# Kernel optimization log

Measured on AMD Instinct MI355X. Metric: run time of the kernel, lower is better.

Reference implementation:

```python
import jax, jax.numpy as jnp
import numpy as np

N, D, C, S = 100000, 512, 4096, 50000


def setup_inputs() -> dict:
    key = jax.random.key(0)
    k1, k2 = jax.random.split(key)
    X = jax.random.normal(k1, (N, D), dtype=jnp.float32)
    codebook_sum = jax.random.normal(k2, (C, D), dtype=jnp.float32)
    prompt_mask = jnp.arange(N) < S  # first S rows are support (True), rest are queries
    return {"X": X, "codebook_sum": codebook_sum, "prompt_mask": prompt_mask, "num_support": S}


def reference(X, codebook_sum, prompt_mask, num_support):
    # num_support is a static Python int (replaces torch.nonzero(prompt_mask) dynamic split)
    s = num_support
    support = X[:s]                                   # [S, D] support (prompt_mask==True)
    query = X[s:]                                     # [Q, D] queries (prompt_mask==False)
    # dense similarity matmul + top-1 nearest-codebook search + gather
    cos_sim = jnp.einsum('sd,cd->sc', support, codebook_sum)  # [S, C]
    top_idx = jnp.argmax(cos_sim, axis=1)             # [S]
    code_n = codebook_sum[top_idx]                    # [S, D] gathered nearest codes
    # mean-pooled prototypes broadcast over queries
    proto = jnp.mean(support, axis=0)                 # [D]
    proto_code = jnp.mean(code_n, axis=0)             # [D]
    # euclidean distances to each prototype
    query_score = jnp.sqrt(jnp.sum((query - proto) ** 2, axis=1))        # [Q]
    query_score_code = jnp.sqrt(jnp.sum((query - proto_code) ** 2, axis=1))  # [Q]
    return (query_score + query_score_code) / 2
```

## Files before the change

kernel.cpp:

```cpp
#include <hip/hip_runtime.h>
#include <hip/hip_bf16.h>

#define NTOT 100000
#define DIM  512
#define CB   4096
#define SSUP 50000
#define NQ   (NTOT - SSUP)

#define MTILES 391
#define MPAD   (MTILES * 128)
#define NTILES 32

typedef __bf16 bf16x8 __attribute__((ext_vector_type(8)));
typedef __bf16 bf16x4 __attribute__((ext_vector_type(4)));
typedef float  f32x4  __attribute__((ext_vector_type(4)));

#define OFF_CBBF   0
#define OFF_XB     4194304
#define OFF_PV     55443456
#define OFF_PI     61849600
#define OFF_PSUM   68255744
#define OFF_PCSUM  68257792
#define OFF_HIST   68259840
#define OFF_TIDX   68276224
#define WS_NEED    (68276224 + 200000)
#define ZERO_BYTES (2048 + 2048 + 16384)

#define F_OFF_PSUM   4194304
#define F_OFF_PCSUM  4196352
#define F_OFF_HIST   4198400
#define F_OFF_TIDX   4214784

__device__ __forceinline__ void load_lds16(const void* g, void* l) {
    __builtin_amdgcn_global_load_lds(
        (const __attribute__((address_space(1))) void*)g,
        (__attribute__((address_space(3))) void*)l, 16, 0, 0);
}

__global__ void k_convert(const float* __restrict__ src, __bf16* __restrict__ dst) {
    int i = (blockIdx.x * 256 + threadIdx.x) * 4;
    float4 v = *(const float4*)(src + i);
    bf16x4 o;
    o[0] = (__bf16)v.x; o[1] = (__bf16)v.y; o[2] = (__bf16)v.z; o[3] = (__bf16)v.w;
    *(bf16x4*)(dst + i) = o;
}

__global__ void k_proto_sum(const float* __restrict__ X, float* __restrict__ protoSum) {
    const int d = threadIdx.x;
    const int r0 = blockIdx.x * 500;
    float acc = 0.f;
    for (int r = r0; r < r0 + 500; ++r)
        acc += X[(size_t)r * DIM + d];
    atomicAdd(&protoSum[d], acc);
}

__global__ __launch_bounds__(256)
void k_gemm_tile(const __bf16* __restrict__ Xb, const __bf16* __restrict__ cbb,
                 float* __restrict__ pv, int* __restrict__ pi)
{
    __shared__ __bf16 lA[128 * 32];
    __shared__ __bf16 lB[128 * 32];
    __shared__ float  sv[128][2];
    __shared__ int    si[128][2];

    const int tid  = threadIdx.x;
    const int wave = tid >> 6;
    const int lane = tid & 63;
    const int wm   = wave >> 1;
    const int wn   = wave & 1;
    const int l15  = lane & 15;
    const int q    = lane >> 4;
    const int nt   = blockIdx.x;
    const int mt   = blockIdx.y;
    const size_t r0 = (size_t)mt * 128;
    const int    c0 = nt * 128;

    f32x4 acc[4][4];
    #pragma unroll
    for (int i = 0; i < 4; ++i)
        #pragma unroll
        for (int j = 0; j < 4; ++j)
            acc[i][j] = (f32x4){0.f, 0.f, 0.f, 0.f};

    for (int k0 = 0; k0 < 512; k0 += 32) {
        __syncthreads();
        #pragma unroll
        for (int i = 0; i < 2; ++i) {
            const int ck  = i * 256 + tid;
            const int row = ck >> 2;
            const int kc  = ck & 3;
            load_lds16(Xb  + (r0 + row) * DIM + k0 + kc * 8, lA + ck * 8);
            load_lds16(cbb + (size_t)(c0 + row) * DIM + k0 + kc * 8, lB + ck * 8);
        }
        __syncthreads();

        bf16x8 af[4], bfr[4];
        #pragma unroll
        for (int t = 0; t < 4; ++t) {
            af[t]  = *(const bf16x8*)(lA + (wm * 64 + t * 16 + l15) * 32 + q * 8);
            bfr[t] = *(const bf16x8*)(lB + (wn * 64 + t * 16 + l15) * 32 + q * 8);
        }
        #pragma unroll
        for (int tm = 0; tm < 4; ++tm)
            #pragma unroll
            for (int tn = 0; tn < 4; ++tn)
                acc[tm][tn] = __builtin_amdgcn_mfma_f32_16x16x32_bf16(
                    af[tm], bfr[tn], acc[tm][tn], 0, 0, 0);
    }

    #pragma unroll
    for (int tm = 0; tm < 4; ++tm) {
        #pragma unroll
        for (int reg = 0; reg < 4; ++reg) {
            float v = -3.0e38f; int idx = 0;
            #pragma unroll
            for (int tn = 0; tn < 4; ++tn) {
                float x = acc[tm][tn][reg];
                int   c = c0 + wn * 64 + tn * 16 + l15;
                if (x > v) { v = x; idx = c; }
            }
            #pragma unroll
            for (int off = 1; off < 16; off <<= 1) {
                float ov = __shfl_xor(v, off, 64);
                int   oi = __shfl_xor(idx, off, 64);
                if (ov > v) { v = ov; idx = oi; }
            }
            if (l15 == 0) {
                int rl = wm * 64 + tm * 16 + q * 4 + reg;
                sv[rl][wn] = v;
                si[rl][wn] = idx;
            }
        }
    }
    __syncthreads();
    if (tid < 128) {
        float v0 = sv[tid][0], v1 = sv[tid][1];
        size_t r = r0 + tid;
        pv[r * 32 + nt] = fmaxf(v0, v1);
        pi[r * 32 + nt] = (v1 > v0) ? si[tid][1] : si[tid][0];
    }
}

__global__ void k_argmax_reduce(const float* __restrict__ pv, const int* __restrict__ pi,
                                int* __restrict__ top_idx) {
    int r = blockIdx.x * 256 + threadIdx.x;
    if (r >= SSUP) return;
    float v = -3.0e38f; int idx = 0;
    #pragma unroll 8
    for (int j = 0; j < 32; ++j) {
        float x = pv[(size_t)r * 32 + j];
        if (x > v) { v = x; idx = pi[(size_t)r * 32 + j]; }
    }
    top_idx[r] = idx;
}

__global__ __launch_bounds__(256, 2)
void k_gemm_argmax(const float* __restrict__ X, const __bf16* __restrict__ cbb,
                   int* __restrict__ top_idx)
{
    __shared__ float redv[64][2];
    __shared__ int   redi[64][2];

    const int tid  = threadIdx.x;
    const int wave = tid >> 6;
    const int lane = tid & 63;
    const int wm   = wave >> 1;
    const int wn   = wave & 1;
    const int l15  = lane & 15;
    const int q    = lane >> 4;
    const int r0   = blockIdx.x * 64;

    bf16x8 aflat[2][16];
    #pragma unroll
    for (int tm = 0; tm < 2; ++tm) {
        const int r = r0 + wm * 32 + tm * 16 + l15;
        const bool valid = (r < SSUP);
        const float* xr = X + (size_t)r * DIM + q * 8;
        #pragma unroll
        for (int kt = 0; kt < 16; ++kt) {
            float4 v0, v1;
            if (valid) {
                v0 = *(const float4*)(xr + kt * 32);
                v1 = *(const float4*)(xr + kt * 32 + 4);
            } else {
                v0 = make_float4(0.f, 0.f, 0.f, 0.f);
                v1 = v0;
            }
            bf16x8 f;
            f[0] = (__bf16)v0.x; f[1] = (__bf16)v0.y; f[2] = (__bf16)v0.z; f[3] = (__bf16)v0.w;
            f[4] = (__bf16)v1.x; f[5] = (__bf16)v1.y; f[6] = (__bf16)v1.z; f[7] = (__bf16)v1.w;
            aflat[tm][kt] = f;
        }
    }

    float mx[8];
    int   mi[8];
    #pragma unroll
    for (int i = 0; i < 8; ++i) { mx[i] = -3.0e38f; mi[i] = 0; }
    const f32x4 zero4 = {0.f, 0.f, 0.f, 0.f};

    for (int ct = 0; ct < 32; ++ct) {
        const int c0 = ct * 128 + wn * 64;
        const __bf16* bptr[4];
        #pragma unroll
        for (int tn = 0; tn < 4; ++tn)
            bptr[tn] = cbb + (size_t)(c0 + tn * 16 + l15) * DIM + q * 8;

        f32x4 acc[2][4];
        #pragma unroll
        for (int i = 0; i < 2; ++i)
            #pragma unroll
            for (int j = 0; j < 4; ++j)
                acc[i][j] = zero4;

        #pragma unroll
        for (int kt = 0; kt < 16; ++kt) {
            bf16x8 b[4];
            #pragma unroll
            for (int tn = 0; tn < 4; ++tn)
                b[tn] = *(const bf16x8*)(bptr[tn] + kt * 32);
            #pragma unroll
            for (int tm = 0; tm < 2; ++tm)
                #pragma unroll
                for (int tn = 0; tn < 4; ++tn)
                    acc[tm][tn] = __builtin_amdgcn_mfma_f32_16x16x32_bf16(
                        aflat[tm][kt], b[tn], acc[tm][tn], 0, 0, 0);
        }
        #pragma unroll
        for (int tm = 0; tm < 2; ++tm)
            #pragma unroll
            for (int tn = 0; tn < 4; ++tn)
                #pragma unroll
                for (int reg = 0; reg < 4; ++reg) {
                    float v = acc[tm][tn][reg];
                    int slot = tm * 4 + reg;
                    int col  = c0 + tn * 16 + l15;
                    if (v > mx[slot]) { mx[slot] = v; mi[slot] = col; }
                }
    }

    #pragma unroll
    for (int slot = 0; slot < 8; ++slot) {
        float v  = mx[slot];
        int  idx = mi[slot];
        #pragma unroll
        for (int off = 1; off < 16; off <<= 1) {
            float ov = __shfl_xor(v, off, 64);
            int   oi = __shfl_xor(idx, off, 64);
            if (ov > v) { v = ov; idx = oi; }
        }
        if (l15 == 0) {
            int rowl = wm * 32 + (slot >> 2) * 16 + q * 4 + (slot & 3);
            redv[rowl][wn] = v;
            redi[rowl][wn] = idx;
        }
    }
    __syncthreads();
    if (tid < 64) {
        int r = r0 + tid;
        if (r < SSUP) {
            float v0 = redv[tid][0], v1 = redv[tid][1];
            top_idx[r] = (v1 > v0) ? redi[tid][1] : redi[tid][0];
        }
    }
}

__global__ void k_hist(const int* __restrict__ top_idx, int* __restrict__ hist) {
    __shared__ int lh[CB];
    for (int i = threadIdx.x; i < CB; i += blockDim.x) lh[i] = 0;
    __syncthreads();
    for (int i = blockIdx.x * blockDim.x + threadIdx.x; i < SSUP; i += gridDim.x * blockDim.x)
        atomicAdd(&lh[top_idx[i]], 1);
    __syncthreads();
    for (int i = threadIdx.x; i < CB; i += blockDim.x) {
        int v = lh[i];
        if (v) atomicAdd(&hist[i], v);
    }
}

__global__ void k_proto_code(const float* __restrict__ cb, const int* __restrict__ hist,
                             float* __restrict__ pcSum) {
    const int d  = threadIdx.x;
    const int c0 = blockIdx.x * 64;
    float acc = 0.f;
    for (int c = c0; c < c0 + 64; ++c) {
        float w = (float)hist[c];
        if (w != 0.f) acc += w * cb[(size_t)c * DIM + d];
    }
    atomicAdd(&pcSum[d], acc);
}

__global__ void k_query(const float* __restrict__ X, const float* __restrict__ protoSum,
                        const float* __restrict__ pcSum, float* __restrict__ out) {
    const int lane   = threadIdx.x & 63;
    const int waveId = (blockIdx.x * blockDim.x + threadIdx.x) >> 6;
    const int nwaves = (gridDim.x * blockDim.x) >> 6;
    const float invS = 1.0f / (float)SSUP;

    for (int r = waveId; r < NQ; r += nwaves) {
        const float* xr = X + (size_t)(SSUP + r) * DIM;
        float s1 = 0.f, s2 = 0.f;
        #pragma unroll
        for (int i = 0; i < 2; ++i) {
            int dd = lane * 4 + i * 256;
            float4 xq = *(const float4*)(xr + dd);
            float4 p  = *(const float4*)(protoSum + dd);
            float4 pc = *(const float4*)(pcSum + dd);
            float d0, d1, d2, d3;
            d0 = xq.x - p.x * invS; d1 = xq.y - p.y * invS;
            d2 = xq.z - p.z * invS; d3 = xq.w - p.w * invS;
            s1 += d0 * d0 + d1 * d1 + d2 * d2 + d3 * d3;
            d0 = xq.x - pc.x * invS; d1 = xq.y - pc.y * invS;
            d2 = xq.z - pc.z * invS; d3 = xq.w - pc.w * invS;
            s2 += d0 * d0 + d1 * d1 + d2 * d2 + d3 * d3;
        }
        #pragma unroll
        for (int off = 32; off > 0; off >>= 1) {
            s1 += __shfl_xor(s1, off, 64);
            s2 += __shfl_xor(s2, off, 64);
        }
        if (lane == 0)
            out[r] = 0.5f * (sqrtf(s1) + sqrtf(s2));
    }
}

extern "C" void kernel_launch(void* const* d_in, const int* in_sizes, int n_in,
                              void* d_out, int out_size, void* d_ws, size_t ws_size,
                              hipStream_t stream) {
    const float* X  = (const float*)d_in[0];
    const float* cb = (const float*)d_in[1];
    float* out = (float*)d_out;
    char* ws = (char*)d_ws;

    __bf16* cbb = (__bf16*)(ws + OFF_CBBF);

    if (ws_size >= (size_t)WS_NEED) {
        __bf16* Xb       = (__bf16*)(ws + OFF_XB);
        float*  pv       = (float*)(ws + OFF_PV);
        int*    pi       = (int*)(ws + OFF_PI);
        float*  protoSum = (float*)(ws + OFF_PSUM);
        float*  pcSum    = (float*)(ws + OFF_PCSUM);
        int*    hist     = (int*)(ws + OFF_HIST);
        int*    top_idx  = (int*)(ws + OFF_TIDX);

        hipMemsetAsync(ws + OFF_PSUM, 0, ZERO_BYTES, stream);

        k_convert<<<(CB * DIM) / 1024, 256, 0, stream>>>(cb, cbb);
        k_convert<<<(MPAD * DIM) / 1024, 256, 0, stream>>>(X, Xb);
        k_proto_sum<<<100, 512, 0, stream>>>(X, protoSum);

        dim3 grid(NTILES, MTILES);
        k_gemm_tile<<<grid, 256, 0, stream>>>(Xb, cbb, pv, pi);

        k_argmax_reduce<<<(SSUP + 255) / 256, 256, 0, stream>>>(pv, pi, top_idx);
        k_hist<<<64, 256, 0, stream>>>(top_idx, hist);
        k_proto_code<<<CB / 64, 512, 0, stream>>>(cb, hist, pcSum);
        k_query<<<1024, 256, 0, stream>>>(X, protoSum, pcSum, out);
    } else {
        float*  protoSum = (float*)(ws + F_OFF_PSUM);
        float*  pcSum    = (float*)(ws + F_OFF_PCSUM);
        int*    hist     = (int*)(ws + F_OFF_HIST);
        int*    top_idx  = (int*)(ws + F_OFF_TIDX);

        hipMemsetAsync(ws + F_OFF_PSUM, 0, ZERO_BYTES, stream);

        k_convert<<<(CB * DIM) / 1024, 256, 0, stream>>>(cb, cbb);
        k_proto_sum<<<100, 512, 0, stream>>>(X, protoSum);
        k_gemm_argmax<<<(SSUP + 63) / 64, 256, 0, stream>>>(X, cbb, top_idx);
        k_hist<<<64, 256, 0, stream>>>(top_idx, hist);
        k_proto_code<<<CB / 64, 512, 0, stream>>>(cb, hist, pcSum);
        k_query<<<1024, 256, 0, stream>>>(X, protoSum, pcSum, out);
    }
}
```

Baseline: 621.9 us.

## Replace GEMM with 256x256 software-pipelined swizzled MFMA kernel and fuse convert+protosum

Replaces the 128x128 single-buffered GEMM with a 256x256-tile, 8-wave kernel. It double-buffers K-slices of 64 in a 128KB LDS using direct global-to-LDS loads with an XOR swizzle, and interleaves loads with MFMA quads under explicit waitcnt and barrier control plus setprio. The bf16 conversion of X is fused with the support-row prototype sum, so X is read once in that stage. The argmax partials shrink to 16 per row. The change aims to raise MFMA utilisation and cut global and LDS traffic, but it adds heavy manual synchronisation and a large LDS footprint that limits occupancy.

```diff
diff --git a/kernel.cpp b/kernel.cpp
--- a/kernel.cpp
+++ b/kernel.cpp
@@ -7,9 +7,9 @@
 #define SSUP 50000
 #define NQ   (NTOT - SSUP)
 
-#define MTILES 391
-#define MPAD   (MTILES * 128)
-#define NTILES 32
+#define MT2   196
+#define MPAD2 (MT2 * 256)
+#define NT2   16
 
 typedef __bf16 bf16x8 __attribute__((ext_vector_type(8)));
 typedef __bf16 bf16x4 __attribute__((ext_vector_type(4)));
@@ -17,13 +17,13 @@
 
 #define OFF_CBBF   0
 #define OFF_XB     4194304
-#define OFF_PV     55443456
-#define OFF_PI     61849600
-#define OFF_PSUM   68255744
-#define OFF_PCSUM  68257792
-#define OFF_HIST   68259840
-#define OFF_TIDX   68276224
-#define WS_NEED    (68276224 + 200000)
+#define OFF_PV     55574528
+#define OFF_PI     58785792
+#define OFF_PSUM   61997056
+#define OFF_PCSUM  61999104
+#define OFF_HIST   62001152
+#define OFF_TIDX   62017536
+#define WS_NEED    (62017536 + 200000)
 #define ZERO_BYTES (2048 + 2048 + 16384)
 
 #define F_OFF_PSUM   4194304
@@ -36,6 +36,11 @@
         (const __attribute__((address_space(1))) void*)g,
         (__attribute__((address_space(3))) void*)l, 16, 0, 0);
 }
+
+#define BARRIER() __builtin_amdgcn_s_barrier()
+#define LGKM0()   do { asm volatile("s_waitcnt lgkmcnt(0)" ::: "memory"); \
+                       __builtin_amdgcn_sched_barrier(0); } while (0)
+#define VMC(N)    asm volatile("s_waitcnt vmcnt(" #N ")" ::: "memory")
 
 __global__ void k_convert(const float* __restrict__ src, __bf16* __restrict__ dst) {
     int i = (blockIdx.x * 256 + threadIdx.x) * 4;
@@ -43,6 +48,287 @@
     bf16x4 o;
     o[0] = (__bf16)v.x; o[1] = (__bf16)v.y; o[2] = (__bf16)v.z; o[3] = (__bf16)v.w;
     *(bf16x4*)(dst + i) = o;
+}
+
+__global__ __launch_bounds__(256)
+void k_conv_psum(const float* __restrict__ X, __bf16* __restrict__ Xb,
+                 float* __restrict__ protoSum)
+{
+    __shared__ float red[4][512];
+    const int tid  = threadIdx.x;
+    const int c8   = (tid & 63) * 8;
+    const int rsub = tid >> 6;
+    const size_t rbase = (size_t)blockIdx.x * 512 + rsub;
+
+    float acc[8];
+    #pragma unroll
+    for (int j = 0; j < 8; ++j) acc[j] = 0.f;
+
+    for (int r = 0; r < 512; r += 4) {
+        const size_t row = rbase + r;
+        const float* p = X + row * DIM + c8;
+        float4 v0 = *(const float4*)p;
+        float4 v1 = *(const float4*)(p + 4);
+        bf16x8 o;
+        o[0] = (__bf16)v0.x; o[1] = (__bf16)v0.y; o[2] = (__bf16)v0.z; o[3] = (__bf16)v0.w;
+        o[4] = (__bf16)v1.x; o[5] = (__bf16)v1.y; o[6] = (__bf16)v1.z; o[7] = (__bf16)v1.w;
+        *(bf16x8*)(Xb + row * DIM + c8) = o;
+        if (row < SSUP) {
+            acc[0] += v0.x; acc[1] += v0.y; acc[2] += v0.z; acc[3] += v0.w;
+            acc[4] += v1.x; acc[5] += v1.y; acc[6] += v1.z; acc[7] += v1.w;
+        }
+    }
+    #pragma unroll
+    for (int j = 0; j < 8; ++j) red[rsub][c8 + j] = acc[j];
+    __syncthreads();
+    if (rsub == 0) {
+        #pragma unroll
+        for (int j = 0; j < 8; ++j)
+            atomicAdd(&protoSum[c8 + j],
+                      red[0][c8 + j] + red[1][c8 + j] + red[2][c8 + j] + red[3][c8 + j]);
+    }
+}
+
+
+__device__ __forceinline__ void stage_half(const __bf16* __restrict__ g, size_t grow0,
+                                           int k0, char* ldsop, int half, int tid)
+{
+    char* dst = ldsop + half * 16384;
+    #pragma unroll
+    for (int i = 0; i < 2; ++i) {
+        const int ck  = i * 512 + tid;
+        const int row = ck >> 3;
+        const int sc  = (ck & 7) ^ (row & 7);
+        load_lds16(g + (grow0 + (size_t)row) * DIM + k0 + sc * 8, dst + ck * 16);
+    }
+}
+
+template<int BUFOFF, int MH>
+__device__ __forceinline__ void ds_load_A(const char* aptr, int off0, int off1,
+                                          bf16x8 (&a)[4][2])
+{
+    #pragma unroll
+    for (int t = 0; t < 4; ++t) {
+        const char* p = aptr + BUFOFF + MH * 8192 + t * 2048;
+        a[t][0] = *(const bf16x8*)(p + off0);
+        a[t][1] = *(const bf16x8*)(p + off1);
+    }
+}
+
+template<int BUFOFF, int NH>
+__device__ __forceinline__ void ds_load_B(const char* bptr, int off0, int off1,
+                                          bf16x8 (&b)[2][2])
+{
+    #pragma unroll
+    for (int n = 0; n < 2; ++n) {
+        const char* p = bptr + BUFOFF + NH * 4096 + n * 2048;
+        b[n][0] = *(const bf16x8*)(p + off0);
+        b[n][1] = *(const bf16x8*)(p + off1);
+    }
+}
+
+template<int MH, int NH>
+__device__ __forceinline__ void mfma_quad(const bf16x8 (&a)[4][2], const bf16x8 (&b)[2][2],
+                                          f32x4 (&acc)[8][4])
+{
+    __builtin_amdgcn_s_setprio(1);
+    #pragma unroll
+    for (int t = 0; t < 4; ++t)
+        #pragma unroll
+        for (int n = 0; n < 2; ++n)
+            #pragma unroll
+            for (int ks = 0; ks < 2; ++ks)
+                acc[MH * 4 + t][NH * 2 + n] = __builtin_amdgcn_mfma_f32_16x16x32_bf16(
+                    a[t][ks], b[n][ks], acc[MH * 4 + t][NH * 2 + n], 0, 0, 0);
+    __builtin_amdgcn_s_setprio(0);
+    __builtin_amdgcn_sched_barrier(0);
+}
+
+__global__ __launch_bounds__(512, 2)
+void k_gemm256(const __bf16* __restrict__ Xb, const __bf16* __restrict__ cbb,
+               float* __restrict__ pv, int* __restrict__ pi)
+{
+    __shared__ __align__(16) char lds[131072];
+
+    const int tid  = threadIdx.x;
+    const int lane = tid & 63;
+    const int wid  = tid >> 6;
+    const int wm   = wid >> 2;
+    const int wn   = wid & 3;
+    const int l15  = lane & 15;
+    const int q    = lane >> 4;
+    const int nt   = blockIdx.x;
+    const int mt   = blockIdx.y;
+    const size_t r0  = (size_t)mt * 256;
+    const size_t c0g = (size_t)nt * 256;
+
+    const int off0 = l15 * 128 + ((q)     ^ (l15 & 7)) * 16;
+    const int off1 = l15 * 128 + ((4 + q) ^ (l15 & 7)) * 16;
+    const char* aptr = lds + wm * 16384;
+    const char* bptr = lds + wn * 8192;
+
+    f32x4 acc[8][4];
+    #pragma unroll
+    for (int i = 0; i < 8; ++i)
+        #pragma unroll
+        for (int j = 0; j < 4; ++j)
+            acc[i][j] = (f32x4){0.f, 0.f, 0.f, 0.f};
+
+    bf16x8 a[4][2], b0[2][2], b1[2][2];
+
+    stage_half(Xb,  r0,        0,  lds + 0,     0, tid);
+    stage_half(Xb,  r0 + 128,  0,  lds + 0,     1, tid);
+    stage_half(cbb, c0g,       0,  lds + 32768, 0, tid);
+    stage_half(cbb, c0g + 128, 0,  lds + 32768, 1, tid);
+    stage_half(cbb, c0g,       64, lds + 98304, 0, tid);
+    stage_half(cbb, c0g + 128, 64, lds + 98304, 1, tid);
+    VMC(4);
+    BARRIER();
+
+    #pragma unroll 1
+    for (int it = 0; it < 3; ++it) {
+        const int kA1 = (2 * it + 1) * 64;
+        const int k2  = (2 * it + 2) * 64;
+        const int kB3 = (2 * it + 3) * 64;
+        ds_load_A<0, 0>(aptr, off0, off1, a);
+        ds_load_B<32768, 0>(bptr, off0, off1, b0);
+        stage_half(Xb, r0, kA1, lds + 65536, 0, tid);
+        BARRIER(); LGKM0();
+        mfma_quad<0, 0>(a, b0, acc);
+        BARRIER();
+        ds_load_B<32768, 1>(bptr, off0, off1, b1);
+        stage_half(Xb, r0 + 128, kA1, lds + 65536, 1, tid);
+        BARRIER(); LGKM0();
+        mfma_quad<0, 1>(a, b1, acc);
+        BARRIER();
+        ds_load_A<0, 1>(aptr, off0, off1, a);
+        stage_half(cbb, c0g, k2, lds + 32768, 0, tid);
+        BARRIER(); LGKM0();
+        mfma_quad<1, 1>(a, b1, acc);
+        BARRIER();
+        stage_half(cbb, c0g + 128, k2, lds + 32768, 1, tid);
+        VMC(4);
+        BARRIER();
+        mfma_quad<1, 0>(a, b0, acc);
+        BARRIER();
+        ds_load_A<65536, 0>(aptr, off0, off1, a);
+        ds_load_B<98304, 0>(bptr, off0, off1, b0);
+        stage_half(Xb, r0, k2, lds + 0, 0, tid);
+        BARRIER(); LGKM0();
+        mfma_quad<0, 0>(a, b0, acc);
+        BARRIER();
+        ds_load_B<98304, 1>(bptr, off0, off1, b1);
+        stage_half(Xb, r0 + 128, k2, lds + 0, 1, tid);
+        BARRIER(); LGKM0();
+        mfma_quad<0, 1>(a, b1, acc);
+        BARRIER();
+        ds_load_A<65536, 1>(aptr, off0, off1, a);
+        stage_half(cbb, c0g, kB3, lds + 98304, 0, tid);
+        BARRIER(); LGKM0();
+        mfma_quad<1, 1>(a, b1, acc);
+        BARRIER();
+        stage_half(cbb, c0g + 128, kB3, lds + 98304, 1, tid);
+        VMC(4);
+        BARRIER();
+        mfma_quad<1, 0>(a, b0, acc);
+        BARRIER();
+    }
+
+    {
+        const int k7 = 7 * 64;
+        ds_load_A<0, 0>(aptr, off0, off1, a);
+        ds_load_B<32768, 0>(bptr, off0, off1, b0);
+        stage_half(Xb, r0, k7, lds + 65536, 0, tid);
+        BARRIER(); LGKM0();
+        mfma_quad<0, 0>(a, b0, acc);
+        BARRIER();
+
+        ds_load_B<32768, 1>(bptr, off0, off1, b1);
+        stage_half(Xb, r0 + 128, k7, lds + 65536, 1, tid);
+        BARRIER(); LGKM0();
+        mfma_quad<0, 1>(a, b1, acc);
+        BARRIER();
+
+        ds_load_A<0, 1>(aptr, off0, off1, a);
+        BARRIER(); LGKM0();
+        mfma_quad<1, 1>(a, b1, acc);
+        BARRIER();
+
+        VMC(0);
+        BARRIER();
+        mfma_quad<1, 0>(a, b0, acc);
+        BARRIER();
+
+        ds_load_A<65536, 0>(aptr, off0, off1, a);
+        ds_load_B<98304, 0>(bptr, off0, off1, b0);
+        BARRIER(); LGKM0();
+        mfma_quad<0, 0>(a, b0, acc);
+        BARRIER();
+
+        ds_load_B<98304, 1>(bptr, off0, off1, b1);
+        BARRIER(); LGKM0();
+        mfma_quad<0, 1>(a, b1, acc);
+        BARRIER();
+
+        ds_load_A<65536, 1>(aptr, off0, off1, a);
+        BARRIER(); LGKM0();
+        mfma_quad<1, 1>(a, b1, acc);
+        BARRIER();
+
+        mfma_quad<1, 0>(a, b0, acc);
+    }
+
+    float* sv = (float*)lds;
+    int*   si = (int*)(lds + 4096);
+    #pragma unroll
+    for (int fm = 0; fm < 8; ++fm) {
+        #pragma unroll
+        for (int reg = 0; reg < 4; ++reg) {
+            float v = -3.0e38f; int idx = 0;
+            #pragma unroll
+            for (int fn = 0; fn < 4; ++fn) {
+                float x = acc[fm][fn][reg];
+                int   c = (int)c0g + wn * 64 + fn * 16 + l15;
+                if (x > v) { v = x; idx = c; }
+            }
+            #pragma unroll
+            for (int off = 1; off < 16; off <<= 1) {
+                float ov = __shfl_xor(v, off, 64);
+                int   oi = __shfl_xor(idx, off, 64);
+                if (ov > v) { v = ov; idx = oi; }
+            }
+            if (l15 == 0) {
+                int rl = wm * 128 + fm * 16 + q * 4 + reg;
+                sv[rl * 4 + wn] = v;
+                si[rl * 4 + wn] = idx;
+            }
+        }
+    }
+    __syncthreads();
+    if (tid < 256) {
+        float v = sv[tid * 4]; int idx = si[tid * 4];
+        #pragma unroll
+        for (int j = 1; j < 4; ++j) {
+            float x = sv[tid * 4 + j];
+            if (x > v) { v = x; idx = si[tid * 4 + j]; }
+        }
+        size_t r = r0 + tid;
+        pv[r * 16 + nt] = v;
+        pi[r * 16 + nt] = idx;
+    }
+}
+
+__global__ void k_argmax_reduce16(const float* __restrict__ pv, const int* __restrict__ pi,
+                                  int* __restrict__ top_idx) {
+    int r = blockIdx.x * 256 + threadIdx.x;
+    if (r >= SSUP) return;
+    float v = -3.0e38f; int idx = 0;
+    #pragma unroll
+    for (int j = 0; j < 16; ++j) {
+        float x = pv[(size_t)r * 16 + j];
+        if (x > v) { v = x; idx = pi[(size_t)r * 16 + j]; }
+    }
+    top_idx[r] = idx;
 }
 
 __global__ void k_proto_sum(const float* __restrict__ X, float* __restrict__ protoSum) {
@@ -52,106 +338,6 @@
     for (int r = r0; r < r0 + 500; ++r)
         acc += X[(size_t)r * DIM + d];
     atomicAdd(&protoSum[d], acc);
-}
-
-__global__ __launch_bounds__(256)
-void k_gemm_tile(const __bf16* __restrict__ Xb, const __bf16* __restrict__ cbb,
-                 float* __restrict__ pv, int* __restrict__ pi)
-{
-    __shared__ __bf16 lA[128 * 32];
-    __shared__ __bf16 lB[128 * 32];
-    __shared__ float  sv[128][2];
-    __shared__ int    si[128][2];
-
-    const int tid  = threadIdx.x;
-    const int wave = tid >> 6;
-    const int lane = tid & 63;
-    const int wm   = wave >> 1;
-    const int wn   = wave & 1;
-    const int l15  = lane & 15;
-    const int q    = lane >> 4;
-    const int nt   = blockIdx.x;
-    const int mt   = blockIdx.y;
-    const size_t r0 = (size_t)mt * 128;
-    const int    c0 = nt * 128;
-
-    f32x4 acc[4][4];
-    #pragma unroll
-    for (int i = 0; i < 4; ++i)
-        #pragma unroll
-        for (int j = 0; j < 4; ++j)
-            acc[i][j] = (f32x4){0.f, 0.f, 0.f, 0.f};
-
-    for (int k0 = 0; k0 < 512; k0 += 32) {
-        __syncthreads();
-        #pragma unroll
-        for (int i = 0; i < 2; ++i) {
-            const int ck  = i * 256 + tid;
-            const int row = ck >> 2;
-            const int kc  = ck & 3;
-            load_lds16(Xb  + (r0 + row) * DIM + k0 + kc * 8, lA + ck * 8);
-            load_lds16(cbb + (size_t)(c0 + row) * DIM + k0 + kc * 8, lB + ck * 8);
-        }
-        __syncthreads();
-
-        bf16x8 af[4], bfr[4];
-        #pragma unroll
-        for (int t = 0; t < 4; ++t) {
-            af[t]  = *(const bf16x8*)(lA + (wm * 64 + t * 16 + l15) * 32 + q * 8);
-            bfr[t] = *(const bf16x8*)(lB + (wn * 64 + t * 16 + l15) * 32 + q * 8);
-        }
-        #pragma unroll
-        for (int tm = 0; tm < 4; ++tm)
-            #pragma unroll
-            for (int tn = 0; tn < 4; ++tn)
-                acc[tm][tn] = __builtin_amdgcn_mfma_f32_16x16x32_bf16(
-                    af[tm], bfr[tn], acc[tm][tn], 0, 0, 0);
-    }
-
-    #pragma unroll
-    for (int tm = 0; tm < 4; ++tm) {
-        #pragma unroll
-        for (int reg = 0; reg < 4; ++reg) {
-            float v = -3.0e38f; int idx = 0;
-            #pragma unroll
-            for (int tn = 0; tn < 4; ++tn) {
-                float x = acc[tm][tn][reg];
-                int   c = c0 + wn * 64 + tn * 16 + l15;
-                if (x > v) { v = x; idx = c; }
-            }
-            #pragma unroll
-            for (int off = 1; off < 16; off <<= 1) {
-                float ov = __shfl_xor(v, off, 64);
-                int   oi = __shfl_xor(idx, off, 64);
-                if (ov > v) { v = ov; idx = oi; }
-            }
-            if (l15 == 0) {
-                int rl = wm * 64 + tm * 16 + q * 4 + reg;
-                sv[rl][wn] = v;
-                si[rl][wn] = idx;
-            }
-        }
-    }
-    __syncthreads();
-    if (tid < 128) {
-        float v0 = sv[tid][0], v1 = sv[tid][1];
-        size_t r = r0 + tid;
-        pv[r * 32 + nt] = fmaxf(v0, v1);
-        pi[r * 32 + nt] = (v1 > v0) ? si[tid][1] : si[tid][0];
-    }
-}
-
-__global__ void k_argmax_reduce(const float* __restrict__ pv, const int* __restrict__ pi,
-                                int* __restrict__ top_idx) {
-    int r = blockIdx.x * 256 + threadIdx.x;
-    if (r >= SSUP) return;
-    float v = -3.0e38f; int idx = 0;
-    #pragma unroll 8
-    for (int j = 0; j < 32; ++j) {
-        float x = pv[(size_t)r * 32 + j];
-        if (x > v) { v = x; idx = pi[(size_t)r * 32 + j]; }
-    }
-    top_idx[r] = idx;
 }
 
 __global__ __launch_bounds__(256, 2)
@@ -346,13 +532,12 @@
         hipMemsetAsync(ws + OFF_PSUM, 0, ZERO_BYTES, stream);
 
         k_convert<<<(CB * DIM) / 1024, 256, 0, stream>>>(cb, cbb);
-        k_convert<<<(MPAD * DIM) / 1024, 256, 0, stream>>>(X, Xb);
-        k_proto_sum<<<100, 512, 0, stream>>>(X, protoSum);
-
-        dim3 grid(NTILES, MTILES);
-        k_gemm_tile<<<grid, 256, 0, stream>>>(Xb, cbb, pv, pi);
-
-        k_argmax_reduce<<<(SSUP + 255) / 256, 256, 0, stream>>>(pv, pi, top_idx);
+        k_conv_psum<<<MPAD2 / 512, 256, 0, stream>>>(X, Xb, protoSum);
+
+        dim3 grid(NT2, MT2);
+        k_gemm256<<<grid, 512, 0, stream>>>(Xb, cbb, pv, pi);
+
+        k_argmax_reduce16<<<(SSUP + 255) / 256, 256, 0, stream>>>(pv, pi, top_idx);
         k_hist<<<64, 256, 0, stream>>>(top_idx, hist);
         k_proto_code<<<CB / 64, 512, 0, stream>>>(cb, hist, pcSum);
         k_query<<<1024, 256, 0, stream>>>(X, protoSum, pcSum, out);
```

Measured after the change: 646.4 us. +3.9%, slower.
